# Kernel tuning notes

Hardware: AMD Instinct MI355X
Metric: run time of the kernel (lower is better)

Reference implementation:

```python
import jax, jax.numpy as jnp
import numpy as np

N = 100000      # nodes (all frames flattened)
E = 1600000     # edges
F_IN = 64       # num_features
H = 32          # hidden_dim (hard-coded in module)
C = 2           # num_classes
G = 500         # number of graphs / temporal frames
BN_EPS = 1e-5


def setup_inputs() -> dict:
    key = jax.random.key(0)
    ks = jax.random.split(key, 16)

    def w(i, shape):
        return jax.random.normal(ks[i], shape, jnp.float32) * 0.1

    z = lambda *s: jnp.zeros(s, jnp.float32)
    o = lambda *s: jnp.ones(s, jnp.float32)

    return {
        "x": jax.random.normal(ks[0], (N, F_IN), jnp.float32),
        "edge_index": jax.random.randint(ks[1], (2, E), 0, N),
        "batch": jnp.sort(jax.random.randint(ks[2], (N,), 0, G)),
        # GINConv 0 MLP: Linear(F_IN,H) -> ReLU -> Linear(H,H)
        "gin0_W1": w(3, (H, F_IN)), "gin0_b1": z(H),
        "gin0_W2": w(4, (H, H)),    "gin0_b2": z(H),
        "bn0_gamma": o(H), "bn0_beta": z(H), "bn0_mean": z(H), "bn0_var": o(H),
        # GINConv 1 MLP: Linear(H,H) -> ReLU -> Linear(H,H)
        "gin1_W1": w(5, (H, H)), "gin1_b1": z(H),
        "gin1_W2": w(6, (H, H)), "gin1_b2": z(H),
        "bn1_gamma": o(H), "bn1_beta": z(H), "bn1_mean": z(H), "bn1_var": o(H),
        # dense tail
        "fc1_W": w(7, (H, H)), "fc1_b": z(H),
        "fc2_W": w(8, (C, H)), "fc2_b": z(C),
        # bidirectional LSTM (input C, hidden H), torch gate order i,f,g,o
        "lstm_Wih_f": w(9, (4 * H, C)),  "lstm_Whh_f": w(10, (4 * H, H)),
        "lstm_bih_f": z(4 * H),          "lstm_bhh_f": z(4 * H),
        "lstm_Wih_b": w(11, (4 * H, C)), "lstm_Whh_b": w(12, (4 * H, H)),
        "lstm_bih_b": z(4 * H),          "lstm_bhh_b": z(4 * H),
        "red_W": w(13, (C, 2 * H)), "red_b": z(C),
    }


def _lstm_final_h(seq, Wih, Whh, bih, bhh):
    # seq: [T, C]; returns final hidden state [H]. torch gate order: i, f, g, o.
    def step(carry, xt):
        h, c = carry
        zg = xt @ Wih.T + bih + h @ Whh.T + bhh
        i, f, g, o = jnp.split(zg, 4)
        c = jax.nn.sigmoid(f) * c + jax.nn.sigmoid(i) * jnp.tanh(g)
        h = jax.nn.sigmoid(o) * jnp.tanh(c)
        return (h, c), None
    init = (jnp.zeros((H,), seq.dtype), jnp.zeros((H,), seq.dtype))
    (h, _), _ = jax.lax.scan(step, init, seq)
    return h


def reference(x, edge_index, batch,
              gin0_W1, gin0_b1, gin0_W2, gin0_b2,
              bn0_gamma, bn0_beta, bn0_mean, bn0_var,
              gin1_W1, gin1_b1, gin1_W2, gin1_b2,
              bn1_gamma, bn1_beta, bn1_mean, bn1_var,
              fc1_W, fc1_b, fc2_W, fc2_b,
              lstm_Wih_f, lstm_Whh_f, lstm_bih_f, lstm_bhh_f,
              lstm_Wih_b, lstm_Whh_b, lstm_bih_b, lstm_bhh_b,
              red_W, red_b):
    src, dst = edge_index[0], edge_index[1]

    def gin(h, W1, b1, W2, b2):
        # GINConv with eps=0: MLP(x_i + sum_{j->i} x_j)
        agg = jax.ops.segment_sum(h[src], dst, num_segments=N) + h
        return jax.nn.relu(agg @ W1.T + b1) @ W2.T + b2

    def bn(h, g, b, m, v):  # BatchNorm1d (eval, running stats)
        return (h - m) * (g / jnp.sqrt(v + BN_EPS)) + b

    h = bn(jax.nn.relu(gin(x, gin0_W1, gin0_b1, gin0_W2, gin0_b2)),
           bn0_gamma, bn0_beta, bn0_mean, bn0_var)
    h = bn(jax.nn.relu(gin(h, gin1_W1, gin1_b1, gin1_W2, gin1_b2)),
           bn1_gamma, bn1_beta, bn1_mean, bn1_var)

    g = jax.ops.segment_sum(h, batch, num_segments=G)      # global_add_pool [G,H]
    g = jax.nn.relu(g @ fc1_W.T + fc1_b)                   # (dropout is eval/no-op)
    seq = g @ fc2_W.T + fc2_b                              # [G, C]

    h_f = _lstm_final_h(seq, lstm_Wih_f, lstm_Whh_f, lstm_bih_f, lstm_bhh_f)
    h_b = _lstm_final_h(seq[::-1], lstm_Wih_b, lstm_Whh_b, lstm_bih_b, lstm_bhh_b)
    out = jax.nn.relu(jnp.concatenate([h_f, h_b]) @ red_W.T + red_b)  # [C]
    return jax.nn.log_softmax(out, axis=-1)
```

## Files before the change

kernel.cpp:

```cpp
#include <hip/hip_runtime.h>
#include <math.h>

#define N_NODES 100000
#define N_EDGES 1600000
#define F_IN    64
#define H       32
#define C       2
#define G       500
#define BN_EPS  1e-5f

#define NPART        8
#define NODES_PER_P  12500
#define EPB          2048

__global__ __launch_bounds__(256) void k_zero_i(int* __restrict__ p, int n) {
    int i = blockIdx.x * 256 + threadIdx.x;
    if (i < n) p[i] = 0;
}

__global__ __launch_bounds__(256) void k_hist(
    const int* __restrict__ ei, int* __restrict__ deg)
{
    int e = blockIdx.x * 256 + threadIdx.x;
    if (e < N_EDGES) atomicAdd(&deg[ei[N_EDGES + e]], 1);
}

__global__ __launch_bounds__(256) void k_scan1(
    int* __restrict__ rowptr, int* __restrict__ bsum)
{
    __shared__ int s[256];
    int i = blockIdx.x * 256 + threadIdx.x;
    int v = (i < N_NODES) ? rowptr[i] : 0;
    s[threadIdx.x] = v;
    __syncthreads();
    for (int off = 1; off < 256; off <<= 1) {
        int t = (threadIdx.x >= off) ? s[threadIdx.x - off] : 0;
        __syncthreads();
        s[threadIdx.x] += t;
        __syncthreads();
    }
    if (i < N_NODES) rowptr[i] = s[threadIdx.x] - v;
    if (threadIdx.x == 255) bsum[blockIdx.x] = s[255];
}

__global__ __launch_bounds__(256) void k_scan3(
    int* __restrict__ rowptr, const int* __restrict__ bsum, int nb,
    int* __restrict__ cursor, float* __restrict__ gpool)
{
    __shared__ int sb[512];
    int tid = threadIdx.x;
    for (int j = tid; j < nb; j += 256) sb[j] = bsum[j];
    __syncthreads();
    if (tid == 0) {
        int run = 0;
        for (int j = 0; j < nb; ++j) { int t = sb[j]; sb[j] = run; run += t; }
    }
    __syncthreads();
    int i = blockIdx.x * 256 + tid;
    if (i < N_NODES) {
        int r = rowptr[i] + sb[i >> 8];
        rowptr[i] = r;
        cursor[i] = r;
    }
    if (i == 0) rowptr[N_NODES] = N_EDGES;
    if (i < G * H) gpool[i] = 0.f;
}

__global__ __launch_bounds__(256) void k_scatter(
    const int* __restrict__ ei, int* __restrict__ cursor,
    int* __restrict__ elist)
{
    int p    = blockIdx.x & (NPART - 1);
    int lo   = p * NODES_PER_P;
    int hi   = lo + NODES_PER_P;
    int base = (blockIdx.x >> 3) * EPB;
    for (int i = threadIdx.x; i < EPB; i += 256) {
        int e = base + i;
        if (e < N_EDGES) {
            int d = ei[N_EDGES + e];
            if (d >= lo && d < hi) {
                int pos = atomicAdd(&cursor[d], 1);
                elist[pos] = ei[e];
            }
        }
    }
}

__global__ __launch_bounds__(256) void k_xform0(
    const float* __restrict__ x, const float* __restrict__ W1,
    float* __restrict__ y)
{
    __shared__ float Wt[F_IN * H];
    __shared__ float xs[8 * F_IN];
    int tid = threadIdx.x;
    for (int idx = tid; idx < F_IN * H; idx += 256) {
        int f = idx & (H - 1);
        int k = idx >> 5;
        Wt[k * H + f] = W1[f * F_IN + k];
    }
    int n0 = blockIdx.x * 8;
    for (int idx = tid; idx < 8 * F_IN; idx += 256) {
        int nl = idx >> 6, k = idx & 63;
        int n = n0 + nl;
        xs[idx] = (n < N_NODES) ? x[n * F_IN + k] : 0.f;
    }
    __syncthreads();
    int nl = tid >> 5, f = tid & 31;
    int n = n0 + nl;
    if (n < N_NODES) {
        float acc = 0.f;
#pragma unroll
        for (int k = 0; k < F_IN; ++k) acc += xs[nl * F_IN + k] * Wt[k * H + f];
        y[n * H + f] = acc;
    }
}

__global__ __launch_bounds__(256) void k_aggmlp0(
    const int* __restrict__ rowptr, const int* __restrict__ elist,
    const float* __restrict__ y,
    const float* __restrict__ b1, const float* __restrict__ W2,
    const float* __restrict__ b2,
    const float* __restrict__ gamma, const float* __restrict__ beta,
    const float* __restrict__ mean,  const float* __restrict__ var,
    const float* __restrict__ nW,
    float* __restrict__ y_out)
{
    __shared__ float W2t[H * H];
    __shared__ float nWt[H * H];
    __shared__ float tb[16][H + 1];
    __shared__ float hb[16][H + 1];
    int tid = threadIdx.x;
    for (int idx = tid; idx < H * H; idx += 256) {
        int f = idx & 31, k = idx >> 5;
        W2t[k * H + f] = W2[f * H + k];
        nWt[k * H + f] = nW[f * H + k];
    }
    int nl = tid >> 4;
    int q  = tid & 15;
    int n  = blockIdx.x * 16 + nl;
    bool ok = n < N_NODES;

    float2 a = make_float2(0.f, 0.f), b = a, c = a, d = a;
    if (ok) {
        int j  = rowptr[n];
        int j1 = rowptr[n + 1];
        const float2* y2 = (const float2*)y;
        a = y2[n * 16 + q];
        for (; j + 4 <= j1; j += 4) {
            int s0 = elist[j],     s1 = elist[j + 1];
            int s2 = elist[j + 2], s3 = elist[j + 3];
            float2 v0 = y2[s0 * 16 + q];
            float2 v1 = y2[s1 * 16 + q];
            float2 v2 = y2[s2 * 16 + q];
            float2 v3 = y2[s3 * 16 + q];
            a.x += v0.x; a.y += v0.y;
            b.x += v1.x; b.y += v1.y;
            c.x += v2.x; c.y += v2.y;
            d.x += v3.x; d.y += v3.y;
        }
        for (; j < j1; ++j) {
            int s0 = elist[j];
            float2 v0 = y2[s0 * 16 + q];
            a.x += v0.x; a.y += v0.y;
        }
        a.x += b.x + c.x + d.x;
        a.y += b.y + c.y + d.y;
    }
    tb[nl][2 * q]     = fmaxf(a.x + b1[2 * q],     0.f);
    tb[nl][2 * q + 1] = fmaxf(a.y + b1[2 * q + 1], 0.f);
    __syncthreads();

    float z0 = b2[q], z1 = b2[q + 16];
#pragma unroll
    for (int k = 0; k < H; ++k) {
        float tk = tb[nl][k];
        z0 = fmaf(tk, W2t[k * H + q],      z0);
        z1 = fmaf(tk, W2t[k * H + q + 16], z1);
    }
    z0 = fmaxf(z0, 0.f);
    z1 = fmaxf(z1, 0.f);
    float s0 = gamma[q]      * rsqrtf(var[q]      + BN_EPS);
    float s1 = gamma[q + 16] * rsqrtf(var[q + 16] + BN_EPS);
    hb[nl][q]      = (z0 - mean[q])      * s0 + beta[q];
    hb[nl][q + 16] = (z1 - mean[q + 16]) * s1 + beta[q + 16];
    __syncthreads();

    float yv0 = 0.f, yv1 = 0.f;
#pragma unroll
    for (int k = 0; k < H; ++k) {
        float hk = hb[nl][k];
        yv0 = fmaf(hk, nWt[k * H + q],      yv0);
        yv1 = fmaf(hk, nWt[k * H + q + 16], yv1);
    }
    if (ok) {
        y_out[n * H + q]      = yv0;
        y_out[n * H + q + 16] = yv1;
    }
}

__global__ __launch_bounds__(256) void k_aggmlp1_pool(
    const int* __restrict__ rowptr, const int* __restrict__ elist,
    const float* __restrict__ y, const int* __restrict__ batch,
    const float* __restrict__ b1, const float* __restrict__ W2,
    const float* __restrict__ b2,
    const float* __restrict__ gamma, const float* __restrict__ beta,
    const float* __restrict__ mean,  const float* __restrict__ var,
    float* __restrict__ gpool)
{
    __shared__ float W2t[H * H];
    __shared__ float tb[16][H + 1];
    __shared__ float hb[16][H + 1];
    __shared__ int   bs[16];
    int tid = threadIdx.x;
    for (int idx = tid; idx < H * H; idx += 256) {
        int f = idx & 31, k = idx >> 5;
        W2t[k * H + f] = W2[f * H + k];
    }
    int nl = tid >> 4;
    int q  = tid & 15;
    int n  = blockIdx.x * 16 + nl;
    bool ok = n < N_NODES;
    if (tid < 16) {
        int nn = blockIdx.x * 16 + tid;
        bs[tid] = (nn < N_NODES) ? batch[nn] : -1;
    }

    float2 a = make_float2(0.f, 0.f), b = a, c = a, d = a;
    if (ok) {
        int j  = rowptr[n];
        int j1 = rowptr[n + 1];
        const float2* y2 = (const float2*)y;
        a = y2[n * 16 + q];
        for (; j + 4 <= j1; j += 4) {
            int s0 = elist[j],     s1 = elist[j + 1];
            int s2 = elist[j + 2], s3 = elist[j + 3];
            float2 v0 = y2[s0 * 16 + q];
            float2 v1 = y2[s1 * 16 + q];
            float2 v2 = y2[s2 * 16 + q];
            float2 v3 = y2[s3 * 16 + q];
            a.x += v0.x; a.y += v0.y;
            b.x += v1.x; b.y += v1.y;
            c.x += v2.x; c.y += v2.y;
            d.x += v3.x; d.y += v3.y;
        }
        for (; j < j1; ++j) {
            int s0 = elist[j];
            float2 v0 = y2[s0 * 16 + q];
            a.x += v0.x; a.y += v0.y;
        }
        a.x += b.x + c.x + d.x;
        a.y += b.y + c.y + d.y;
    }
    tb[nl][2 * q]     = fmaxf(a.x + b1[2 * q],     0.f);
    tb[nl][2 * q + 1] = fmaxf(a.y + b1[2 * q + 1], 0.f);
    __syncthreads();

    float z0 = b2[q], z1 = b2[q + 16];
#pragma unroll
    for (int k = 0; k < H; ++k) {
        float tk = tb[nl][k];
        z0 = fmaf(tk, W2t[k * H + q],      z0);
        z1 = fmaf(tk, W2t[k * H + q + 16], z1);
    }
    z0 = fmaxf(z0, 0.f);
    z1 = fmaxf(z1, 0.f);
    float s0 = gamma[q]      * rsqrtf(var[q]      + BN_EPS);
    float s1 = gamma[q + 16] * rsqrtf(var[q + 16] + BN_EPS);
    hb[nl][q]      = (z0 - mean[q])      * s0 + beta[q];
    hb[nl][q + 16] = (z1 - mean[q + 16]) * s1 + beta[q + 16];
    __syncthreads();

    if (ok && (nl == 0 || bs[nl] != bs[nl - 1])) {
        int bid = bs[nl];
        float acc0 = hb[nl][q];
        float acc1 = hb[nl][q + 16];
        for (int j = nl + 1; j < 16 && bs[j] == bid; ++j) {
            acc0 += hb[j][q];
            acc1 += hb[j][q + 16];
        }
        atomicAdd(&gpool[bid * H + q],      acc0);
        atomicAdd(&gpool[bid * H + q + 16], acc1);
    }
}

__global__ __launch_bounds__(256) void k_fc(
    const float* __restrict__ gpool,
    const float* __restrict__ fc1W, const float* __restrict__ fc1b,
    const float* __restrict__ fc2W, const float* __restrict__ fc2b,
    float* __restrict__ seq)
{
    __shared__ float W1t[H * H];
    __shared__ float gs[8][H];
    __shared__ float tb[8][H];
    int tid = threadIdx.x;
    for (int idx = tid; idx < H * H; idx += 256) {
        int f = idx & 31, k = idx >> 5;
        W1t[k * H + f] = fc1W[f * H + k];
    }
    int n0 = blockIdx.x * 8;
    int nl = tid >> 5, f = tid & 31;
    int g = n0 + nl;
    bool ok = g < G;
    gs[nl][f] = ok ? gpool[g * H + f] : 0.f;
    __syncthreads();
    float z = fc1b[f];
#pragma unroll
    for (int k = 0; k < H; ++k) z += gs[nl][k] * W1t[k * H + f];
    tb[nl][f] = fmaxf(z, 0.f);
    __syncthreads();
    if (ok && f < C) {
        float z2 = fc2b[f];
#pragma unroll
        for (int k = 0; k < H; ++k) z2 += tb[nl][k] * fc2W[f * H + k];
        seq[g * C + f] = z2;
    }
}


#if __has_builtin(__builtin_amdgcn_readlane)
#define RDL(v, k) __int_as_float(__builtin_amdgcn_readlane(__float_as_int(v), (k)))
#else
#define RDL(v, k) __shfl((v), (k), 64)
#endif

#define LOG2E  1.4426950408889634f
#define N2L2E  2.8853900817779268f

#if __has_builtin(__builtin_amdgcn_exp2f) && __has_builtin(__builtin_amdgcn_rcpf)
#define EXP2F(x) __builtin_amdgcn_exp2f(x)
#define RCPF(x)  __builtin_amdgcn_rcpf(x)
#else
#define EXP2F(x) exp2f(x)
#define RCPF(x)  (1.f / (x))
#endif

__device__ __forceinline__ float fsig(float x) {
    return RCPF(1.f + EXP2F(-LOG2E * x));
}
__device__ __forceinline__ float ftanh(float x) {
    return 2.f * RCPF(1.f + EXP2F(-N2L2E * x)) - 1.f;
}

#define PIN4(v) asm("" : "+v"((v).x), "+v"((v).y), "+v"((v).z), "+v"((v).w))

#define SPLIT(d_lo, d_hi, src)                                            \
    asm("v_mov_b32 %0, %2\n\t"                                            \
        "v_mov_b32 %1, %2\n\t"                                            \
        "v_permlane32_swap_b32 %0, %1"                                    \
        : "=&v"(d_lo), "=&v"(d_hi)                                        \
        : "v"(src));

#define ACC4_(av, bv, hA, hB, hC, hD)                                     \
    z0 = fmaf((av).x, hA, z0); z1 = fmaf((av).y, hB, z1);                 \
    z2 = fmaf((av).z, hC, z2); z3 = fmaf((av).w, hD, z3);                 \
    y0 = fmaf((bv).x, hA, y0); y1 = fmaf((bv).y, hB, y1);                 \
    y2 = fmaf((bv).z, hC, y2); y3 = fmaf((bv).w, hD, y3);

__global__ __launch_bounds__(128, 1) void k_lstm(
    const float* __restrict__ seq,
    const float* __restrict__ Wih_f, const float* __restrict__ Whh_f,
    const float* __restrict__ bih_f, const float* __restrict__ bhh_f,
    const float* __restrict__ Wih_b, const float* __restrict__ Whh_b,
    const float* __restrict__ bih_b, const float* __restrict__ bhh_b,
    const float* __restrict__ redW, const float* __restrict__ redb,
    float* __restrict__ out)
{
    __shared__ float  sq[G * C];
    __shared__ float  hl[2][H];
    __shared__ float4 wl4[2048];
    int tid  = threadIdx.x;
    int dir  = tid >> 6;
    int lane = tid & 63;

    for (int i = tid; i < G * C; i += 128) sq[i] = seq[i];
    for (int i = tid; i < 2048; i += 128) {
        int d  = i >> 10;
        int r  = i & 1023;
        int ab = r >> 9;
        int k4 = (r >> 6) & 7;
        int l  = r & 63;
        const float4* src4 = (const float4*)(d ? Whh_b : Whh_f);
        wl4[i] = src4[(ab * 64 + l) * 8 + k4];
    }
    __syncthreads();

    const float* Wih = dir ? Wih_b : Wih_f;
    const float* bih = dir ? bih_b : bih_f;
    const float* bhh = dir ? bhh_b : bhh_f;

    int ra = lane;
    int rb = lane + 64;

    const float4* wA = &wl4[dir * 1024];
    const float4* wB = &wl4[dir * 1024 + 512];

    float4 a0 = wA[0 * 64 + lane], a1 = wA[1 * 64 + lane];
    float4 a2 = wA[2 * 64 + lane], a3 = wA[3 * 64 + lane];
    float4 a4 = wA[4 * 64 + lane], a5 = wA[5 * 64 + lane];
    float4 a6 = wA[6 * 64 + lane], a7 = wA[7 * 64 + lane];
    float4 b0 = wB[0 * 64 + lane], b1 = wB[1 * 64 + lane];
    float4 b2 = wB[2 * 64 + lane], b3 = wB[3 * 64 + lane];
    float4 b4 = wB[4 * 64 + lane], b5 = wB[5 * 64 + lane];
    float4 b6 = wB[6 * 64 + lane], b7 = wB[7 * 64 + lane];
    PIN4(a0); PIN4(a1); PIN4(a2); PIN4(a3);
    PIN4(a4); PIN4(a5); PIN4(a6); PIN4(a7);
    PIN4(b0); PIN4(b1); PIN4(b2); PIN4(b3);
    PIN4(b4); PIN4(b5); PIN4(b6); PIN4(b7);

    float wia0 = Wih[ra * C], wia1 = Wih[ra * C + 1];
    float wib0 = Wih[rb * C], wib1 = Wih[rb * C + 1];
    float bza  = bih[ra] + bhh[ra];
    float bzb  = bih[rb] + bhh[rb];

    float hval = 0.f;
    float cst  = 0.f;

    int tt0 = dir ? (G - 1) : 0;
    float x0 = sq[tt0 * C];
    float x1 = sq[tt0 * C + 1];

#pragma unroll 2
    for (int t = 0; t < G; ++t) {
        int tn = (t + 1 < G) ? (dir ? (G - 2 - t) : (t + 1)) : 0;
        float nx0 = sq[tn * C];
        float nx1 = sq[tn * C + 1];

        float h0  = RDL(hval, 0),  h1  = RDL(hval, 1);
        float h2  = RDL(hval, 2),  h3  = RDL(hval, 3);
        float h4  = RDL(hval, 4),  h5  = RDL(hval, 5);
        float h6  = RDL(hval, 6),  h7  = RDL(hval, 7);
        float h8  = RDL(hval, 8),  h9  = RDL(hval, 9);
        float h10 = RDL(hval, 10), h11 = RDL(hval, 11);
        float h12 = RDL(hval, 12), h13 = RDL(hval, 13);
        float h14 = RDL(hval, 14), h15 = RDL(hval, 15);
        float h16 = RDL(hval, 16), h17 = RDL(hval, 17);
        float h18 = RDL(hval, 18), h19 = RDL(hval, 19);
        float h20 = RDL(hval, 20), h21 = RDL(hval, 21);
        float h22 = RDL(hval, 22), h23 = RDL(hval, 23);
        float h24 = RDL(hval, 24), h25 = RDL(hval, 25);
        float h26 = RDL(hval, 26), h27 = RDL(hval, 27);
        float h28 = RDL(hval, 28), h29 = RDL(hval, 29);
        float h30 = RDL(hval, 30), h31 = RDL(hval, 31);

        float z0 = 0.f, z1 = 0.f, z2 = 0.f, z3 = 0.f;
        float y0 = 0.f, y1 = 0.f, y2 = 0.f, y3 = 0.f;
        ACC4_(a0, b0, h0,  h1,  h2,  h3);
        ACC4_(a1, b1, h4,  h5,  h6,  h7);
        ACC4_(a2, b2, h8,  h9,  h10, h11);
        ACC4_(a3, b3, h12, h13, h14, h15);
        ACC4_(a4, b4, h16, h17, h18, h19);
        ACC4_(a5, b5, h20, h21, h22, h23);
        ACC4_(a6, b6, h24, h25, h26, h27);
        ACC4_(a7, b7, h28, h29, h30, h31);

        float za = bza + fmaf(wia0, x0, fmaf(wia1, x1, (z0 + z1) + (z2 + z3)));
        float zb = bzb + fmaf(wib0, x0, fmaf(wib1, x1, (y0 + y1) + (y2 + y3)));

        float zi, zf, zg, zo;
        SPLIT(zi, zf, za);
        SPLIT(zg, zo, zb);

        cst  = fsig(zf) * cst + fsig(zi) * ftanh(zg);
        hval = fsig(zo) * ftanh(cst);

        x0 = nx0; x1 = nx1;
    }

    if (lane < H) hl[dir][lane] = hval;
    __syncthreads();

    if (tid == 0) {
        float v0 = redb[0], v1 = redb[1];
        for (int k = 0; k < H; ++k) {
            v0 += hl[0][k] * redW[k]         + hl[1][k] * redW[H + k];
            v1 += hl[0][k] * redW[2 * H + k] + hl[1][k] * redW[3 * H + k];
        }
        v0 = fmaxf(v0, 0.f);
        v1 = fmaxf(v1, 0.f);
        float m = fmaxf(v0, v1);
        float l = logf(expf(v0 - m) + expf(v1 - m));
        out[0] = v0 - m - l;
        out[1] = v1 - m - l;
    }
}

extern "C" void kernel_launch(void* const* d_in, const int* in_sizes, int n_in,
                              void* d_out, int out_size, void* d_ws, size_t ws_size,
                              hipStream_t stream) {
    const float* x        = (const float*)d_in[0];
    const int*   ei       = (const int*)  d_in[1];
    const int*   batch    = (const int*)  d_in[2];
    const float* gin0_W1  = (const float*)d_in[3];
    const float* gin0_b1  = (const float*)d_in[4];
    const float* gin0_W2  = (const float*)d_in[5];
    const float* gin0_b2  = (const float*)d_in[6];
    const float* bn0_g    = (const float*)d_in[7];
    const float* bn0_b    = (const float*)d_in[8];
    const float* bn0_m    = (const float*)d_in[9];
    const float* bn0_v    = (const float*)d_in[10];
    const float* gin1_W1  = (const float*)d_in[11];
    const float* gin1_b1  = (const float*)d_in[12];
    const float* gin1_W2  = (const float*)d_in[13];
    const float* gin1_b2  = (const float*)d_in[14];
    const float* bn1_g    = (const float*)d_in[15];
    const float* bn1_b    = (const float*)d_in[16];
    const float* bn1_m    = (const float*)d_in[17];
    const float* bn1_v    = (const float*)d_in[18];
    const float* fc1_W    = (const float*)d_in[19];
    const float* fc1_b    = (const float*)d_in[20];
    const float* fc2_W    = (const float*)d_in[21];
    const float* fc2_b    = (const float*)d_in[22];
    const float* Wih_f    = (const float*)d_in[23];
    const float* Whh_f    = (const float*)d_in[24];
    const float* bih_f    = (const float*)d_in[25];
    const float* bhh_f    = (const float*)d_in[26];
    const float* Wih_b    = (const float*)d_in[27];
    const float* Whh_b    = (const float*)d_in[28];
    const float* bih_b    = (const float*)d_in[29];
    const float* bhh_b    = (const float*)d_in[30];
    const float* red_W    = (const float*)d_in[31];
    const float* red_b    = (const float*)d_in[32];

    float* ws    = (float*)d_ws;
    float* A     = ws;
    float* B     = A + (size_t)N_NODES * H;
    float* gpool = B + (size_t)N_NODES * H;
    float* seq   = gpool + (size_t)G * H;
    int*   rowptr = (int*)(seq + (size_t)G * C);
    int*   cursor = rowptr + (N_NODES + 1);
    int*   bsum   = cursor + N_NODES;
    int*   elist  = bsum + 1024;

    int nblk_nodes   = (N_NODES + 7) / 8;
    int nblk_edges   = (N_EDGES + 255) / 256;
    int nblk_scan    = (N_NODES + 255) / 256;
    int nblk_fuse    = (N_NODES + 15) / 16;
    int nblk_scatter = ((N_EDGES + EPB - 1) / EPB) * NPART;

    k_zero_i<<<nblk_scan, 256, 0, stream>>>(rowptr, N_NODES);
    k_hist<<<nblk_edges, 256, 0, stream>>>(ei, rowptr);
    k_scan1<<<nblk_scan, 256, 0, stream>>>(rowptr, bsum);
    k_scan3<<<nblk_scan, 256, 0, stream>>>(rowptr, bsum, nblk_scan, cursor, gpool);
    k_scatter<<<nblk_scatter, 256, 0, stream>>>(ei, cursor, elist);

    k_xform0<<<nblk_nodes, 256, 0, stream>>>(x, gin0_W1, A);
    k_aggmlp0<<<nblk_fuse, 256, 0, stream>>>(rowptr, elist, A,
                                             gin0_b1, gin0_W2, gin0_b2,
                                             bn0_g, bn0_b, bn0_m, bn0_v,
                                             gin1_W1, B);
    k_aggmlp1_pool<<<nblk_fuse, 256, 0, stream>>>(rowptr, elist, B, batch,
                                                  gin1_b1, gin1_W2, gin1_b2,
                                                  bn1_g, bn1_b, bn1_m, bn1_v,
                                                  gpool);
    k_fc<<<(G + 7) / 8, 256, 0, stream>>>(gpool, fc1_W, fc1_b, fc2_W, fc2_b, seq);
    k_lstm<<<1, 128, 0, stream>>>(seq, Wih_f, Whh_f, bih_f, bhh_f,
                                  Wih_b, Whh_b, bih_b, bhh_b,
                                  red_W, red_b, (float*)d_out);
}
```

Baseline: 451.2 us.

## Fuse degree histogram with first linear transform; use 32 lanes per node

Merges the edge-degree histogram kernel and the x@W1 transform into one launch, with the block index choosing which branch a block runs. This removes one launch and lets the two independent workloads overlap. The aggregation+MLP kernels now handle 8 nodes per block with 32 lanes per node doing scalar float loads, instead of 16 nodes with 16 lanes doing float2 loads. That doubles the block count and the per-block weight-staging overhead, and it changes gather width and per-lane work.

```diff
diff --git a/kernel.cpp b/kernel.cpp
--- a/kernel.cpp
+++ b/kernel.cpp
@@ -18,11 +18,39 @@
     if (i < n) p[i] = 0;
 }
 
-__global__ __launch_bounds__(256) void k_hist(
-    const int* __restrict__ ei, int* __restrict__ deg)
-{
-    int e = blockIdx.x * 256 + threadIdx.x;
-    if (e < N_EDGES) atomicAdd(&deg[ei[N_EDGES + e]], 1);
+__global__ __launch_bounds__(256) void k_histx(
+    const int* __restrict__ ei, int* __restrict__ deg,
+    const float* __restrict__ x, const float* __restrict__ W1,
+    float* __restrict__ y, int nblk_x)
+{
+    __shared__ float Wt[F_IN * H];
+    __shared__ float xs[8 * F_IN];
+    int tid = threadIdx.x;
+    if ((int)blockIdx.x >= nblk_x) {
+        int e = ((int)blockIdx.x - nblk_x) * 256 + tid;
+        if (e < N_EDGES) atomicAdd(&deg[ei[N_EDGES + e]], 1);
+        return;
+    }
+    for (int idx = tid; idx < F_IN * H; idx += 256) {
+        int f = idx & (H - 1);
+        int k = idx >> 5;
+        Wt[k * H + f] = W1[f * F_IN + k];
+    }
+    int n0 = blockIdx.x * 8;
+    for (int idx = tid; idx < 8 * F_IN; idx += 256) {
+        int nl = idx >> 6, k = idx & 63;
+        int n = n0 + nl;
+        xs[idx] = (n < N_NODES) ? x[n * F_IN + k] : 0.f;
+    }
+    __syncthreads();
+    int nl = tid >> 5, f = tid & 31;
+    int n = n0 + nl;
+    if (n < N_NODES) {
+        float acc = 0.f;
+#pragma unroll
+        for (int k = 0; k < F_IN; ++k) acc += xs[nl * F_IN + k] * Wt[k * H + f];
+        y[n * H + f] = acc;
+    }
 }
 
 __global__ __launch_bounds__(256) void k_scan1(
@@ -86,35 +114,6 @@
     }
 }
 
-__global__ __launch_bounds__(256) void k_xform0(
-    const float* __restrict__ x, const float* __restrict__ W1,
-    float* __restrict__ y)
-{
-    __shared__ float Wt[F_IN * H];
-    __shared__ float xs[8 * F_IN];
-    int tid = threadIdx.x;
-    for (int idx = tid; idx < F_IN * H; idx += 256) {
-        int f = idx & (H - 1);
-        int k = idx >> 5;
-        Wt[k * H + f] = W1[f * F_IN + k];
-    }
-    int n0 = blockIdx.x * 8;
-    for (int idx = tid; idx < 8 * F_IN; idx += 256) {
-        int nl = idx >> 6, k = idx & 63;
-        int n = n0 + nl;
-        xs[idx] = (n < N_NODES) ? x[n * F_IN + k] : 0.f;
-    }
-    __syncthreads();
-    int nl = tid >> 5, f = tid & 31;
-    int n = n0 + nl;
-    if (n < N_NODES) {
-        float acc = 0.f;
-#pragma unroll
-        for (int k = 0; k < F_IN; ++k) acc += xs[nl * F_IN + k] * Wt[k * H + f];
-        y[n * H + f] = acc;
-    }
-}
-
 __global__ __launch_bounds__(256) void k_aggmlp0(
     const int* __restrict__ rowptr, const int* __restrict__ elist,
     const float* __restrict__ y,
@@ -127,75 +126,50 @@
 {
     __shared__ float W2t[H * H];
     __shared__ float nWt[H * H];
-    __shared__ float tb[16][H + 1];
-    __shared__ float hb[16][H + 1];
+    __shared__ float tb[8][H + 1];
+    __shared__ float hb[8][H + 1];
     int tid = threadIdx.x;
     for (int idx = tid; idx < H * H; idx += 256) {
         int f = idx & 31, k = idx >> 5;
         W2t[k * H + f] = W2[f * H + k];
         nWt[k * H + f] = nW[f * H + k];
     }
-    int nl = tid >> 4;
-    int q  = tid & 15;
-    int n  = blockIdx.x * 16 + nl;
+    int nl = tid >> 5;
+    int q  = tid & 31;
+    int n  = blockIdx.x * 8 + nl;
     bool ok = n < N_NODES;
 
-    float2 a = make_float2(0.f, 0.f), b = a, c = a, d = a;
+    float a = 0.f, b = 0.f, c = 0.f, d = 0.f;
     if (ok) {
         int j  = rowptr[n];
         int j1 = rowptr[n + 1];
-        const float2* y2 = (const float2*)y;
-        a = y2[n * 16 + q];
+        a = y[n * H + q];
         for (; j + 4 <= j1; j += 4) {
             int s0 = elist[j],     s1 = elist[j + 1];
             int s2 = elist[j + 2], s3 = elist[j + 3];
-            float2 v0 = y2[s0 * 16 + q];
-            float2 v1 = y2[s1 * 16 + q];
-            float2 v2 = y2[s2 * 16 + q];
-            float2 v3 = y2[s3 * 16 + q];
-            a.x += v0.x; a.y += v0.y;
-            b.x += v1.x; b.y += v1.y;
-            c.x += v2.x; c.y += v2.y;
-            d.x += v3.x; d.y += v3.y;
+            a += y[s0 * H + q];
+            b += y[s1 * H + q];
+            c += y[s2 * H + q];
+            d += y[s3 * H + q];
         }
-        for (; j < j1; ++j) {
-            int s0 = elist[j];
-            float2 v0 = y2[s0 * 16 + q];
-            a.x += v0.x; a.y += v0.y;
-        }
-        a.x += b.x + c.x + d.x;
-        a.y += b.y + c.y + d.y;
-    }
-    tb[nl][2 * q]     = fmaxf(a.x + b1[2 * q],     0.f);
-    tb[nl][2 * q + 1] = fmaxf(a.y + b1[2 * q + 1], 0.f);
-    __syncthreads();
-
-    float z0 = b2[q], z1 = b2[q + 16];
+        for (; j < j1; ++j) a += y[elist[j] * H + q];
+        a += b + c + d;
+    }
+    tb[nl][q] = fmaxf(a + b1[q], 0.f);
+    __syncthreads();
+
+    float z = b2[q];
 #pragma unroll
-    for (int k = 0; k < H; ++k) {
-        float tk = tb[nl][k];
-        z0 = fmaf(tk, W2t[k * H + q],      z0);
-        z1 = fmaf(tk, W2t[k * H + q + 16], z1);
-    }
-    z0 = fmaxf(z0, 0.f);
-    z1 = fmaxf(z1, 0.f);
-    float s0 = gamma[q]      * rsqrtf(var[q]      + BN_EPS);
-    float s1 = gamma[q + 16] * rsqrtf(var[q + 16] + BN_EPS);
-    hb[nl][q]      = (z0 - mean[q])      * s0 + beta[q];
-    hb[nl][q + 16] = (z1 - mean[q + 16]) * s1 + beta[q + 16];
-    __syncthreads();
-
-    float yv0 = 0.f, yv1 = 0.f;
+    for (int k = 0; k < H; ++k) z = fmaf(tb[nl][k], W2t[k * H + q], z);
+    z = fmaxf(z, 0.f);
+    float s = gamma[q] * rsqrtf(var[q] + BN_EPS);
+    hb[nl][q] = (z - mean[q]) * s + beta[q];
+    __syncthreads();
+
+    float yv = 0.f;
 #pragma unroll
-    for (int k = 0; k < H; ++k) {
-        float hk = hb[nl][k];
-        yv0 = fmaf(hk, nWt[k * H + q],      yv0);
-        yv1 = fmaf(hk, nWt[k * H + q + 16], yv1);
-    }
-    if (ok) {
-        y_out[n * H + q]      = yv0;
-        y_out[n * H + q + 16] = yv1;
-    }
+    for (int k = 0; k < H; ++k) yv = fmaf(hb[nl][k], nWt[k * H + q], yv);
+    if (ok) y_out[n * H + q] = yv;
 }
 
 __global__ __launch_bounds__(256) void k_aggmlp1_pool(
@@ -208,78 +182,55 @@
     float* __restrict__ gpool)
 {
     __shared__ float W2t[H * H];
-    __shared__ float tb[16][H + 1];
-    __shared__ float hb[16][H + 1];
-    __shared__ int   bs[16];
+    __shared__ float tb[8][H + 1];
+    __shared__ float hb[8][H + 1];
+    __shared__ int   bs[8];
     int tid = threadIdx.x;
     for (int idx = tid; idx < H * H; idx += 256) {
         int f = idx & 31, k = idx >> 5;
         W2t[k * H + f] = W2[f * H + k];
     }
-    int nl = tid >> 4;
-    int q  = tid & 15;
-    int n  = blockIdx.x * 16 + nl;
+    int nl = tid >> 5;
+    int q  = tid & 31;
+    int n  = blockIdx.x * 8 + nl;
     bool ok = n < N_NODES;
-    if (tid < 16) {
-        int nn = blockIdx.x * 16 + tid;
+    if (tid < 8) {
+        int nn = blockIdx.x * 8 + tid;
         bs[tid] = (nn < N_NODES) ? batch[nn] : -1;
     }
 
-    float2 a = make_float2(0.f, 0.f), b = a, c = a, d = a;
+    float a = 0.f, b = 0.f, c = 0.f, d = 0.f;
     if (ok) {
         int j  = rowptr[n];
         int j1 = rowptr[n + 1];
-        const float2* y2 = (const float2*)y;
-        a = y2[n * 16 + q];
+        a = y[n * H + q];
         for (; j + 4 <= j1; j += 4) {
             int s0 = elist[j],     s1 = elist[j + 1];
             int s2 = elist[j + 2], s3 = elist[j + 3];
-            float2 v0 = y2[s0 * 16 + q];
-            float2 v1 = y2[s1 * 16 + q];
-            float2 v2 = y2[s2 * 16 + q];
-            float2 v3 = y2[s3 * 16 + q];
-            a.x += v0.x; a.y += v0.y;
-            b.x += v1.x; b.y += v1.y;
-            c.x += v2.x; c.y += v2.y;
-            d.x += v3.x; d.y += v3.y;
+            a += y[s0 * H + q];
+            b += y[s1 * H + q];
+            c += y[s2 * H + q];
+            d += y[s3 * H + q];
         }
-        for (; j < j1; ++j) {
-            int s0 = elist[j];
-            float2 v0 = y2[s0 * 16 + q];
-            a.x += v0.x; a.y += v0.y;
-        }
-        a.x += b.x + c.x + d.x;
-        a.y += b.y + c.y + d.y;
-    }
-    tb[nl][2 * q]     = fmaxf(a.x + b1[2 * q],     0.f);
-    tb[nl][2 * q + 1] = fmaxf(a.y + b1[2 * q + 1], 0.f);
-    __syncthreads();
-
-    float z0 = b2[q], z1 = b2[q + 16];
+        for (; j < j1; ++j) a += y[elist[j] * H + q];
+        a += b + c + d;
+    }
+    tb[nl][q] = fmaxf(a + b1[q], 0.f);
+    __syncthreads();
+
+    float z = b2[q];
 #pragma unroll
-    for (int k = 0; k < H; ++k) {
-        float tk = tb[nl][k];
-        z0 = fmaf(tk, W2t[k * H + q],      z0);
-        z1 = fmaf(tk, W2t[k * H + q + 16], z1);
-    }
-    z0 = fmaxf(z0, 0.f);
-    z1 = fmaxf(z1, 0.f);
-    float s0 = gamma[q]      * rsqrtf(var[q]      + BN_EPS);
-    float s1 = gamma[q + 16] * rsqrtf(var[q + 16] + BN_EPS);
-    hb[nl][q]      = (z0 - mean[q])      * s0 + beta[q];
-    hb[nl][q + 16] = (z1 - mean[q + 16]) * s1 + beta[q + 16];
+    for (int k = 0; k < H; ++k) z = fmaf(tb[nl][k], W2t[k * H + q], z);
+    z = fmaxf(z, 0.f);
+    float s = gamma[q] * rsqrtf(var[q] + BN_EPS);
+    hb[nl][q] = (z - mean[q]) * s + beta[q];
     __syncthreads();
 
     if (ok && (nl == 0 || bs[nl] != bs[nl - 1])) {
         int bid = bs[nl];
-        float acc0 = hb[nl][q];
-        float acc1 = hb[nl][q + 16];
-        for (int j = nl + 1; j < 16 && bs[j] == bid; ++j) {
-            acc0 += hb[j][q];
-            acc1 += hb[j][q + 16];
-        }
-        atomicAdd(&gpool[bid * H + q],      acc0);
-        atomicAdd(&gpool[bid * H + q + 16], acc1);
+        float acc = hb[nl][q];
+        for (int j = nl + 1; j < 8 && bs[j] == bid; ++j) acc += hb[j][q];
+        atomicAdd(&gpool[bid * H + q], acc);
     }
 }
 
@@ -531,19 +482,19 @@
     int*   bsum   = cursor + N_NODES;
     int*   elist  = bsum + 1024;
 
-    int nblk_nodes   = (N_NODES + 7) / 8;
+    int nblk_x       = (N_NODES + 7) / 8;
     int nblk_edges   = (N_EDGES + 255) / 256;
     int nblk_scan    = (N_NODES + 255) / 256;
-    int nblk_fuse    = (N_NODES + 15) / 16;
+    int nblk_fuse    = (N_NODES + 7) / 8;
     int nblk_scatter = ((N_EDGES + EPB - 1) / EPB) * NPART;
 
     k_zero_i<<<nblk_scan, 256, 0, stream>>>(rowptr, N_NODES);
-    k_hist<<<nblk_edges, 256, 0, stream>>>(ei, rowptr);
+    k_histx<<<nblk_x + nblk_edges, 256, 0, stream>>>(ei, rowptr, x, gin0_W1,
+                                                     A, nblk_x);
     k_scan1<<<nblk_scan, 256, 0, stream>>>(rowptr, bsum);
     k_scan3<<<nblk_scan, 256, 0, stream>>>(rowptr, bsum, nblk_scan, cursor, gpool);
     k_scatter<<<nblk_scatter, 256, 0, stream>>>(ei, cursor, elist);
 
-    k_xform0<<<nblk_nodes, 256, 0, stream>>>(x, gin0_W1, A);
     k_aggmlp0<<<nblk_fuse, 256, 0, stream>>>(rowptr, elist, A,
                                              gin0_b1, gin0_W2, gin0_b2,
                                              bn0_g, bn0_b, bn0_m, bn0_v,
```

Result: slower. 486.9 us (+7.9%).
